# Optimization experiments

Measured on AMD Instinct MI355X. Metric: run time of the kernel, lower is better.

Reference implementation:

```python
import math
import jax, jax.numpy as jnp
import numpy as np

B, T, D, H, FACTOR = 8, 4096, 1024, 16, 5
DH = D // H


def setup_inputs() -> dict:
    key = jax.random.key(0)
    ks = jax.random.split(key, 7)
    u = max(1, min(int(FACTOR * math.log(T + 1)), T))  # = 41
    s = 1.0 / np.sqrt(D).astype(np.float32)
    x = jax.random.normal(ks[0], (B, T, D), jnp.float32)
    Wq = jax.random.normal(ks[1], (D, D), jnp.float32) * s
    Wk = jax.random.normal(ks[2], (D, D), jnp.float32) * s
    Wv = jax.random.normal(ks[3], (D, D), jnp.float32) * s
    Wo = jax.random.normal(ks[4], (D, D), jnp.float32) * s
    bo = jax.random.normal(ks[5], (D,), jnp.float32) * 0.01
    # unique indices, mirroring torch.randperm(T)[:u]
    idx = jax.random.permutation(ks[6], T)[:u].astype(jnp.int32)
    return {"x": x, "Wq": Wq, "Wk": Wk, "Wv": Wv, "Wo": Wo, "bo": bo, "idx": idx}


def reference(x, Wq, Wk, Wv, Wo, bo, idx):
    Bx, Tx, Dx = x.shape
    scale = 1.0 / np.sqrt(DH).astype(np.float32)

    def proj(W):  # torch Linear: x @ W.T, then split heads -> [B,H,T,Dh]
        return (x @ W.T).reshape(Bx, Tx, H, DH).transpose(0, 2, 1, 3)

    Q = proj(Wq)
    K = proj(Wk)
    V = proj(Wv)

    Qs = Q[:, :, idx, :]                                   # [B,H,u,Dh] gather
    scores = jnp.einsum('bhud,bhtd->bhut', Qs, K) * scale  # [B,H,u,T]
    attn = jax.nn.softmax(scores, axis=-1)
    ctx = jnp.einsum('bhut,bhtd->bhud', attn, V)           # [B,H,u,Dh]

    # mean over the u sampled positions fills non-sampled slots
    out = jnp.broadcast_to(ctx.mean(axis=2, keepdims=True), (Bx, H, Tx, DH))
    out = out.at[:, :, idx, :].set(ctx)                    # scatter ctx back

    y = out.transpose(0, 2, 1, 3).reshape(Bx, Tx, Dx)
    return y @ Wo.T + bo
```

## Files before the change

### kernel.cpp

```cpp
#include <hip/hip_runtime.h>
#include <hip/hip_bf16.h>

#define B_  8
#define T_  4096
#define D_  1024
#define H_  16
#define DH_ 64
#define NC_ 4

typedef __bf16 bf8 __attribute__((ext_vector_type(8)));
typedef float f32x4 __attribute__((ext_vector_type(4)));

__device__ __forceinline__ unsigned short f2bf_rn(float f) {
    unsigned u = __float_as_uint(f);
    unsigned r = (u + 0x7FFF + ((u >> 16) & 1)) >> 16;
    return (unsigned short)r;
}

__device__ __forceinline__ void async_load16(const void* gp, void* lp) {
    __builtin_amdgcn_global_load_lds(
        (const __attribute__((address_space(1))) unsigned*)(gp),
        (__attribute__((address_space(3))) unsigned*)(lp), 16, 0, 0);
}

__global__ void k_prep(const float* __restrict__ x, short* __restrict__ xb,
                       const float* __restrict__ Wv, short* __restrict__ Wvb,
                       short* __restrict__ Qtb, const int* __restrict__ idx,
                       int* __restrict__ sel, int U, int HU, int MP, int nzp) {
    int g = blockIdx.x;
    int tid = threadIdx.x;
    if (g < 16896) {
        const float* src = (g < 16384) ? x : Wv;
        short* dst = (g < 16384) ? xb : Wvb;
        size_t gg = (g < 16384) ? g : (g - 16384);
        size_t i = (gg * 256 + tid) * 8;
        float4 a = *(const float4*)(src + i);
        float4 b = *(const float4*)(src + i + 4);
        short4 s0, s1;
        s0.x = (short)f2bf_rn(a.x); s0.y = (short)f2bf_rn(a.y);
        s0.z = (short)f2bf_rn(a.z); s0.w = (short)f2bf_rn(a.w);
        s1.x = (short)f2bf_rn(b.x); s1.y = (short)f2bf_rn(b.y);
        s1.z = (short)f2bf_rn(b.z); s1.w = (short)f2bf_rn(b.w);
        *(short4*)(dst + i) = s0;
        *(short4*)(dst + i + 4) = s1;
    } else if (g < 16896 + nzp) {
        int bi = g - 16896;
        int npad = MP - HU;
        int b = bi / npad, r = bi - b * npad;
        short4 z = {0, 0, 0, 0};
        *(short4*)(Qtb + ((size_t)b * MP + HU + r) * D_ + tid * 4) = z;
    } else {
        for (int t = tid; t < T_; t += 256) sel[t] = 0;
        __syncthreads();
        if (tid < U) sel[idx[tid]] = tid + 1;
    }
}

__global__ __launch_bounds__(256) void k_projg(const float* __restrict__ x,
                                               const int* __restrict__ idx,
                                               const float* __restrict__ W,
                                               float* __restrict__ C, int U) {
    __shared__ float As[32][64 + 4];
    __shared__ float Bs[32][64 + 4];
    __shared__ int sidx[64];
    int M = B_ * U;
    if (threadIdx.x < U) sidx[threadIdx.x] = idx[threadIdx.x];
    __syncthreads();
    int m0 = blockIdx.x * 64, n0 = blockIdx.y * 64;
    int tid = threadIdx.x;
    int lr = tid >> 3, lc = (tid & 7) * 4;
    int ty = tid >> 4, tx = tid & 15;
    float acc[4][4] = {{0.f}};
    for (int k0 = 0; k0 < D_; k0 += 32) {
#pragma unroll
        for (int half = 0; half < 2; ++half) {
            int r = lr + half * 32;
            int gm = m0 + r;
            float4 v = make_float4(0.f, 0.f, 0.f, 0.f);
            if (gm < M) {
                int b = gm / U, i = gm - b * U;
                v = *(const float4*)(x + ((size_t)(b * T_ + sidx[i])) * D_ + k0 + lc);
            }
            As[lc + 0][r] = v.x; As[lc + 1][r] = v.y; As[lc + 2][r] = v.z; As[lc + 3][r] = v.w;
            int gn = n0 + r;
            float4 w = *(const float4*)(W + (size_t)gn * D_ + k0 + lc);
            Bs[lc + 0][r] = w.x; Bs[lc + 1][r] = w.y; Bs[lc + 2][r] = w.z; Bs[lc + 3][r] = w.w;
        }
        __syncthreads();
#pragma unroll
        for (int kk = 0; kk < 32; ++kk) {
            float4 a = *(const float4*)&As[kk][ty * 4];
            float4 bb = *(const float4*)&Bs[kk][tx * 4];
            acc[0][0] += a.x * bb.x; acc[0][1] += a.x * bb.y; acc[0][2] += a.x * bb.z; acc[0][3] += a.x * bb.w;
            acc[1][0] += a.y * bb.x; acc[1][1] += a.y * bb.y; acc[1][2] += a.y * bb.z; acc[1][3] += a.y * bb.w;
            acc[2][0] += a.z * bb.x; acc[2][1] += a.z * bb.y; acc[2][2] += a.z * bb.z; acc[2][3] += a.z * bb.w;
            acc[3][0] += a.w * bb.x; acc[3][1] += a.w * bb.y; acc[3][2] += a.w * bb.z; acc[3][3] += a.w * bb.w;
        }
        __syncthreads();
    }
#pragma unroll
    for (int i = 0; i < 4; ++i) {
        int gm = m0 + ty * 4 + i;
        if (gm < M)
            *(float4*)(C + (size_t)gm * D_ + n0 + tx * 4) =
                make_float4(acc[i][0], acc[i][1], acc[i][2], acc[i][3]);
    }
}

__global__ __launch_bounds__(256) void k_proj(const float* __restrict__ A,
                                              const float* __restrict__ W,
                                              const float* __restrict__ bias,
                                              float* __restrict__ C, int M) {
    __shared__ float As[32][64 + 4];
    __shared__ float Bs[32][64 + 4];
    int m0 = blockIdx.x * 64, n0 = blockIdx.y * 64;
    int tid = threadIdx.x;
    int lr = tid >> 3, lc = (tid & 7) * 4;
    int ty = tid >> 4, tx = tid & 15;
    float acc[4][4] = {{0.f}};
    for (int k0 = 0; k0 < D_; k0 += 32) {
#pragma unroll
        for (int half = 0; half < 2; ++half) {
            int r = lr + half * 32;
            int gm = m0 + r;
            float4 v = make_float4(0.f, 0.f, 0.f, 0.f);
            if (gm < M) v = *(const float4*)(A + (size_t)gm * D_ + k0 + lc);
            As[lc + 0][r] = v.x; As[lc + 1][r] = v.y; As[lc + 2][r] = v.z; As[lc + 3][r] = v.w;
            int gn = n0 + r;
            float4 w = *(const float4*)(W + (size_t)gn * D_ + k0 + lc);
            Bs[lc + 0][r] = w.x; Bs[lc + 1][r] = w.y; Bs[lc + 2][r] = w.z; Bs[lc + 3][r] = w.w;
        }
        __syncthreads();
#pragma unroll
        for (int kk = 0; kk < 32; ++kk) {
            float4 a = *(const float4*)&As[kk][ty * 4];
            float4 bb = *(const float4*)&Bs[kk][tx * 4];
            acc[0][0] += a.x * bb.x; acc[0][1] += a.x * bb.y; acc[0][2] += a.x * bb.z; acc[0][3] += a.x * bb.w;
            acc[1][0] += a.y * bb.x; acc[1][1] += a.y * bb.y; acc[1][2] += a.y * bb.z; acc[1][3] += a.y * bb.w;
            acc[2][0] += a.z * bb.x; acc[2][1] += a.z * bb.y; acc[2][2] += a.z * bb.z; acc[2][3] += a.z * bb.w;
            acc[3][0] += a.w * bb.x; acc[3][1] += a.w * bb.y; acc[3][2] += a.w * bb.z; acc[3][3] += a.w * bb.w;
        }
        __syncthreads();
    }
#pragma unroll
    for (int i = 0; i < 4; ++i) {
        int gm = m0 + ty * 4 + i;
        if (gm < M) {
            int gn = n0 + tx * 4;
            float4 v = make_float4(acc[i][0], acc[i][1], acc[i][2], acc[i][3]);
            if (bias) {
                v.x += bias[gn + 0]; v.y += bias[gn + 1];
                v.z += bias[gn + 2]; v.w += bias[gn + 3];
            }
            *(float4*)(C + (size_t)gm * D_ + gn) = v;
        }
    }
}

__global__ __launch_bounds__(256) void k_qth(const float* __restrict__ Qs,
                                             const float* __restrict__ Wk,
                                             short* __restrict__ Qtb, int U, int MP) {
    __shared__ float As[32][64 + 4];
    __shared__ float Bs[32][64 + 4];
    int h = blockIdx.z;
    int m0 = blockIdx.x * 64, n0 = blockIdx.y * 64;
    int BU = B_ * U;
    int tid = threadIdx.x;
    int lr = tid >> 3, lc = (tid & 7) * 4;
    int ty = tid >> 4, tx = tid & 15;
    float acc[4][4] = {{0.f}};
    for (int k0 = 0; k0 < DH_; k0 += 32) {
#pragma unroll
        for (int half = 0; half < 2; ++half) {
            int r = lr + half * 32;
            int gm = m0 + r;
            float4 v = make_float4(0.f, 0.f, 0.f, 0.f);
            if (gm < BU) v = *(const float4*)(Qs + (size_t)gm * D_ + h * DH_ + k0 + lc);
            As[lc + 0][r] = v.x; As[lc + 1][r] = v.y; As[lc + 2][r] = v.z; As[lc + 3][r] = v.w;
            int kr = (tid >> 4) + half * 16;
            int nc = (tid & 15) * 4;
            float4 w = *(const float4*)(Wk + ((size_t)(h * DH_ + k0 + kr)) * D_ + n0 + nc);
            *(float4*)&Bs[kr][nc] = w;
        }
        __syncthreads();
#pragma unroll
        for (int kk = 0; kk < 32; ++kk) {
            float4 a = *(const float4*)&As[kk][ty * 4];
            float4 bb = *(const float4*)&Bs[kk][tx * 4];
            acc[0][0] += a.x * bb.x; acc[0][1] += a.x * bb.y; acc[0][2] += a.x * bb.z; acc[0][3] += a.x * bb.w;
            acc[1][0] += a.y * bb.x; acc[1][1] += a.y * bb.y; acc[1][2] += a.y * bb.z; acc[1][3] += a.y * bb.w;
            acc[2][0] += a.z * bb.x; acc[2][1] += a.z * bb.y; acc[2][2] += a.z * bb.z; acc[2][3] += a.z * bb.w;
            acc[3][0] += a.w * bb.x; acc[3][1] += a.w * bb.y; acc[3][2] += a.w * bb.z; acc[3][3] += a.w * bb.w;
        }
        __syncthreads();
    }
#pragma unroll
    for (int i = 0; i < 4; ++i) {
        int gm = m0 + ty * 4 + i;
        if (gm < BU) {
            int b = gm / U, ii = gm - b * U;
            short4 s;
            s.x = (short)f2bf_rn(0.125f * acc[i][0]);
            s.y = (short)f2bf_rn(0.125f * acc[i][1]);
            s.z = (short)f2bf_rn(0.125f * acc[i][2]);
            s.w = (short)f2bf_rn(0.125f * acc[i][3]);
            *(short4*)(Qtb + ((size_t)b * MP + h * U + ii) * D_ + n0 + tx * 4) = s;
        }
    }
}

__global__ __launch_bounds__(256) void k_scores_v(const short* __restrict__ Qtb,
                                                  const short* __restrict__ xb,
                                                  const short* __restrict__ Wvb,
                                                  short* __restrict__ attnb,
                                                  short* __restrict__ Vt, int MP) {
    __shared__ short smem[8192];
    short* As = smem;
    short* Bs = smem + 4096;
    int g = blockIdx.x;
    int tid = threadIdx.x;
    int lane = tid & 63, w = tid >> 6;
    int wr = w >> 1, wc = w & 1;
    int quad = lane >> 4, l15 = lane & 15;
    const int K = D_;

    f32x4 acc[4][4];
#pragma unroll
    for (int mi = 0; mi < 4; ++mi)
#pragma unroll
        for (int ni = 0; ni < 4; ++ni)
            acc[mi][ni] = (f32x4){0.f, 0.f, 0.f, 0.f};

    int arow = wr * 64 + l15;
    int brow = wc * 64 + l15;
    int koff = quad * 8;

    if (g < 2048) {
        int mr = g & 7, n = (g >> 3) & 7, mq = g >> 6;
        int m = mq * 8 + mr;
        const short* Ab = xb + (size_t)m * 128 * K;
        const short* Bb = Wvb + (size_t)n * 128 * K;
        for (int kt = 0; kt < K; kt += 32) {
#pragma unroll
            for (int i = 0; i < 2; ++i) {
                int li = i * 256 + tid;
                int row = li >> 2, kc = (li & 3) << 3;
                async_load16(Ab + (size_t)row * K + kt + kc, As + li * 8);
                async_load16(Bb + (size_t)row * K + kt + kc, Bs + li * 8);
            }
            __syncthreads();
            bf8 af[4], bfr[4];
#pragma unroll
            for (int mi = 0; mi < 4; ++mi)
                af[mi] = *(const bf8*)(As + (arow + mi * 16) * 32 + koff);
#pragma unroll
            for (int ni = 0; ni < 4; ++ni)
                bfr[ni] = *(const bf8*)(Bs + (brow + ni * 16) * 32 + koff);
#pragma unroll
            for (int mi = 0; mi < 4; ++mi)
#pragma unroll
                for (int ni = 0; ni < 4; ++ni)
                    acc[mi][ni] = __builtin_amdgcn_mfma_f32_16x16x32_bf16(af[mi], bfr[ni], acc[mi][ni], 0, 0, 0);
            __syncthreads();
        }
        int b = m >> 5;
        int tG0 = (m & 31) * 128 + wr * 64;
        int h = n * 2 + wc;
        short* ep = smem + w * 2048;
        const int PITCH = 80;
#pragma unroll
        for (int ni = 0; ni < 4; ++ni) {
#pragma unroll
            for (int mi = 0; mi < 4; ++mi) {
                short4 s;
                s.x = (short)f2bf_rn(acc[mi][ni][0]);
                s.y = (short)f2bf_rn(acc[mi][ni][1]);
                s.z = (short)f2bf_rn(acc[mi][ni][2]);
                s.w = (short)f2bf_rn(acc[mi][ni][3]);
                *(short4*)(ep + l15 * PITCH + mi * 16 + quad * 4) = s;
            }
#pragma unroll
            for (int it = 0; it < 2; ++it) {
                int dhl = it * 8 + (lane >> 3);
                int seg = lane & 7;
                bf8 v = *(const bf8*)(ep + dhl * PITCH + seg * 8);
                int dh = ni * 16 + dhl;
                *(bf8*)(Vt + ((size_t)(b * H_ + h) * DH_ + dh) * T_ + tG0 + seg * 8) = v;
            }
        }
    } else {
        int gs = g - 2048;
        int n8 = (gs >> 3) & 3;
        int m = (gs >> 5) % 6;
        int b = (gs >> 5) / 6;
        int n = (gs & 7) + 8 * n8;
        const short* Ab = Qtb + (size_t)b * MP * K;
        const short* Bb = xb + (size_t)b * T_ * K;
        short* Cb = attnb + (size_t)b * MP * T_;
        int m0 = m * 128, n0 = n * 128;
        for (int kt = 0; kt < K; kt += 32) {
#pragma unroll
            for (int i = 0; i < 2; ++i) {
                int li = i * 256 + tid;
                int row = li >> 2, kc = (li & 3) << 3;
                async_load16(Ab + (size_t)(m0 + row) * K + kt + kc, As + li * 8);
                async_load16(Bb + (size_t)(n0 + row) * K + kt + kc, Bs + li * 8);
            }
            __syncthreads();
            bf8 af[4], bfr[4];
#pragma unroll
            for (int mi = 0; mi < 4; ++mi)
                af[mi] = *(const bf8*)(As + (arow + mi * 16) * 32 + koff);
#pragma unroll
            for (int ni = 0; ni < 4; ++ni)
                bfr[ni] = *(const bf8*)(Bs + (brow + ni * 16) * 32 + koff);
#pragma unroll
            for (int ni = 0; ni < 4; ++ni)
#pragma unroll
                for (int mi = 0; mi < 4; ++mi)
                    acc[ni][mi] = __builtin_amdgcn_mfma_f32_16x16x32_bf16(bfr[ni], af[mi], acc[ni][mi], 0, 0, 0);
            __syncthreads();
        }
#pragma unroll
        for (int ni = 0; ni < 4; ++ni)
#pragma unroll
            for (int mi = 0; mi < 4; ++mi) {
                int grow = m0 + wr * 64 + mi * 16 + l15;
                int col = n0 + wc * 64 + ni * 16 + quad * 4;
                short4 s;
                s.x = (short)f2bf_rn(__expf(acc[ni][mi][0]));
                s.y = (short)f2bf_rn(__expf(acc[ni][mi][1]));
                s.z = (short)f2bf_rn(__expf(acc[ni][mi][2]));
                s.w = (short)f2bf_rn(__expf(acc[ni][mi][3]));
                *(short4*)(Cb + (size_t)grow * T_ + col) = s;
            }
    }
}

__global__ __launch_bounds__(256) void k_pv(const short* __restrict__ attnb,
                                            const short* __restrict__ Vt,
                                            float* __restrict__ Op,
                                            float* __restrict__ rsp,
                                            int U, int MP) {
    __shared__ short vt[64 * 136];
    int gid = blockIdx.x;
    int c = gid & (NC_ - 1);
    int bh = gid >> 2;
    int h = bh & (H_ - 1);
    int b = bh >> 4;
    int tid = threadIdx.x;
    int lane = tid & 63, w = tid >> 6;
    int quad = lane >> 4;
    const short* Arow = attnb + ((size_t)b * MP + h * U) * T_;
    const short* Vrow = Vt + (size_t)bh * DH_ * T_;

    f32x4 O[3];
#pragma unroll
    for (int mi = 0; mi < 3; ++mi) O[mi] = (f32x4){0.f, 0.f, 0.f, 0.f};
    float rs[3] = {0.f, 0.f, 0.f};

    for (int tt = 0; tt < (T_ / NC_) / 128; ++tt) {
        int t0 = c * (T_ / NC_) + tt * 128;
#pragma unroll
        for (int it = 0; it < 4; ++it) {
            int idx = it * 256 + tid;
            int dh = idx >> 4, seg = idx & 15;
            bf8 v = *(const bf8*)(Vrow + (size_t)dh * T_ + t0 + seg * 8);
            *(bf8*)(vt + dh * 136 + seg * 8) = v;
        }
        __syncthreads();
        bf8 af[3][4];
#pragma unroll
        for (int mi = 0; mi < 3; ++mi)
#pragma unroll
            for (int kf = 0; kf < 4; ++kf)
                af[mi][kf] = *(const bf8*)(Arow + (size_t)(mi * 16 + (lane & 15)) * T_ + t0 + kf * 32 + quad * 8);
        if (w == 0) {
#pragma unroll
            for (int mi = 0; mi < 3; ++mi)
#pragma unroll
                for (int kf = 0; kf < 4; ++kf)
#pragma unroll
                    for (int j = 0; j < 8; ++j) rs[mi] += (float)af[mi][kf][j];
        }
#pragma unroll
        for (int kf = 0; kf < 4; ++kf) {
            bf8 bfr = *(const bf8*)(vt + (w * 16 + (lane & 15)) * 136 + kf * 32 + quad * 8);
#pragma unroll
            for (int mi = 0; mi < 3; ++mi)
                O[mi] = __builtin_amdgcn_mfma_f32_16x16x32_bf16(af[mi][kf], bfr, O[mi], 0, 0, 0);
        }
        __syncthreads();
    }
#pragma unroll
    for (int mi = 0; mi < 3; ++mi)
#pragma unroll
        for (int r = 0; r < 4; ++r)
            Op[((size_t)gid * 48 + mi * 16 + quad * 4 + r) * DH_ + w * 16 + (lane & 15)] = O[mi][r];
    if (w == 0) {
#pragma unroll
        for (int mi = 0; mi < 3; ++mi) {
            rs[mi] += __shfl_xor(rs[mi], 16);
            rs[mi] += __shfl_xor(rs[mi], 32);
            if (quad == 0) rsp[(size_t)gid * 48 + mi * 16 + lane] = rs[mi];
        }
    }
}

__global__ __launch_bounds__(256) void k_rows2(const float* __restrict__ Op,
                                               const float* __restrict__ rsp,
                                               float* __restrict__ R, int U) {
    __shared__ float inv[48];
    __shared__ float msum[4][64];
    int bh = blockIdx.x;
    int b = bh >> 4, h = bh & (H_ - 1);
    int tid = threadIdx.x;
    if (tid < 48) {
        float s = 0.f;
        for (int cc = 0; cc < NC_; ++cc) s += rsp[(size_t)(bh * NC_ + cc) * 48 + tid];
        inv[tid] = 1.f / s;
    }
    __syncthreads();
    int dh = tid & 63, ig = tid >> 6;
    float acc = 0.f;
    for (int p = 0; p < 11; ++p) {
        int i = p * 4 + ig;
        if (i < U) {
            float o = 0.f;
            for (int cc = 0; cc < NC_; ++cc)
                o += Op[((size_t)(bh * NC_ + cc) * 48 + i) * DH_ + dh];
            float v = o * inv[i];
            R[((size_t)b * (U + 1) + 1 + i) * D_ + h * DH_ + dh] = v;
            acc += v;
        }
    }
    msum[ig][dh] = acc;
    __syncthreads();
    if (ig == 0)
        R[((size_t)b * (U + 1)) * D_ + h * DH_ + dh] =
            (msum[0][dh] + msum[1][dh] + msum[2][dh] + msum[3][dh]) / (float)U;
}

__global__ __launch_bounds__(256) void k_fill(const float* __restrict__ Yr,
                                              const int* __restrict__ sel,
                                              float* __restrict__ y, int U) {
    int blk = blockIdx.x;
    int b = blk >> 12, t = blk & (T_ - 1);
    int j = sel[t];
    const float4* src = (const float4*)(Yr + ((size_t)b * (U + 1) + j) * D_);
    float4* dst = (float4*)(y + (size_t)blk * D_);
    dst[threadIdx.x] = src[threadIdx.x];
}

extern "C" void kernel_launch(void* const* d_in, const int* in_sizes, int n_in,
                              void* d_out, int out_size, void* d_ws, size_t ws_size,
                              hipStream_t stream) {
    const float* x  = (const float*)d_in[0];
    const float* Wq = (const float*)d_in[1];
    const float* Wk = (const float*)d_in[2];
    const float* Wv = (const float*)d_in[3];
    const float* Wo = (const float*)d_in[4];
    const float* bo = (const float*)d_in[5];
    const int*  idx = (const int*)d_in[6];
    int U = in_sizes[6];
    int HU = H_ * U;
    int MP = ((HU + 127) / 128) * 128;
    int nzp = B_ * (MP - HU);

    char* w = (char*)d_ws;
    auto alloc = [&](size_t bytes) { char* p = w; w += (bytes + 255) & ~(size_t)255; return p; };

    float* Qs    = (float*)alloc((size_t)B_ * U * D_ * 4);
    short* Qtb   = (short*)alloc((size_t)B_ * MP * D_ * 2);
    short* xb    = (short*)alloc((size_t)B_ * T_ * D_ * 2);
    short* Wvb   = (short*)alloc((size_t)D_ * D_ * 2);
    short* attnb = (short*)alloc((size_t)B_ * MP * T_ * 2);
    short* Vtb   = (short*)alloc((size_t)B_ * D_ * T_ * 2);
    float* Opb   = (float*)alloc((size_t)B_ * H_ * NC_ * 48 * DH_ * 4);
    float* rspb  = (float*)alloc((size_t)B_ * H_ * NC_ * 48 * 4);
    float* R     = (float*)alloc((size_t)B_ * (U + 1) * D_ * 4);
    float* Yr    = (float*)alloc((size_t)B_ * (U + 1) * D_ * 4);
    int*   sel   = (int*)alloc((size_t)T_ * 4);

    k_prep<<<dim3(16896 + nzp + 1), dim3(256), 0, stream>>>(x, xb, Wv, Wvb, Qtb, idx, sel, U, HU, MP, nzp);
    k_projg<<<dim3((B_ * U + 63) / 64, D_ / 64), dim3(256), 0, stream>>>(x, idx, Wq, Qs, U);
    k_qth<<<dim3((B_ * U + 63) / 64, D_ / 64, H_), dim3(256), 0, stream>>>(Qs, Wk, Qtb, U, MP);
    k_scores_v<<<dim3(2048 + 8 * 4 * 6 * B_), dim3(256), 0, stream>>>(Qtb, xb, Wvb, attnb, Vtb, MP);
    k_pv<<<dim3(B_ * H_ * NC_), dim3(256), 0, stream>>>(attnb, Vtb, Opb, rspb, U, MP);
    k_rows2<<<dim3(B_ * H_), dim3(256), 0, stream>>>(Opb, rspb, R, U);
    k_proj<<<dim3((B_ * (U + 1) + 63) / 64, D_ / 64), dim3(256), 0, stream>>>(R, Wo, bo, Yr, B_ * (U + 1));
    k_fill<<<dim3(B_ * T_), dim3(256), 0, stream>>>(Yr, sel, (float*)d_out, U);
}
```

Before: 596.5 us.

## Fuse PV and row normalization into one split-K-per-wave kernel, remap block order

Replaces the chunked k_pv plus k_rows2 pair with a single k_pvT kernel per (batch, head). Its four waves split the 128-wide T tile along K, stage V and P in shared memory, and reduce the partial accumulators and row sums through LDS before writing normalized rows and the mean row directly. This drops one launch and the Op/rsp global round trip. The trade-off is only 128 blocks, down from 512, each walking the full T. It also reorders block indexing in k_scores_v so batch is the fastest-varying index, and changes the epilogue LDS pitch from 80 to 72.

```diff
diff --git a/kernel.cpp b/kernel.cpp
--- a/kernel.cpp
+++ b/kernel.cpp
@@ -6,7 +6,6 @@
 #define D_  1024
 #define H_  16
 #define DH_ 64
-#define NC_ 4
 
 typedef __bf16 bf8 __attribute__((ext_vector_type(8)));
 typedef float f32x4 __attribute__((ext_vector_type(4)));
@@ -236,9 +235,10 @@
     int koff = quad * 8;
 
     if (g < 2048) {
-        int mr = g & 7, n = (g >> 3) & 7, mq = g >> 6;
-        int m = mq * 8 + mr;
-        const short* Ab = xb + (size_t)m * 128 * K;
+        int b = g & 7;
+        int n = (g >> 3) & 7;
+        int mq = g >> 6;
+        const short* Ab = xb + (size_t)(b * 32 + mq) * 128 * K;
         const short* Bb = Wvb + (size_t)n * 128 * K;
         for (int kt = 0; kt < K; kt += 32) {
 #pragma unroll
@@ -263,11 +263,10 @@
                     acc[mi][ni] = __builtin_amdgcn_mfma_f32_16x16x32_bf16(af[mi], bfr[ni], acc[mi][ni], 0, 0, 0);
             __syncthreads();
         }
-        int b = m >> 5;
-        int tG0 = (m & 31) * 128 + wr * 64;
+        int tG0 = mq * 128 + wr * 64;
         int h = n * 2 + wc;
         short* ep = smem + w * 2048;
-        const int PITCH = 80;
+        const int PITCH = 72;
 #pragma unroll
         for (int ni = 0; ni < 4; ++ni) {
 #pragma unroll
@@ -290,10 +289,10 @@
         }
     } else {
         int gs = g - 2048;
-        int n8 = (gs >> 3) & 3;
-        int m = (gs >> 5) % 6;
-        int b = (gs >> 5) / 6;
-        int n = (gs & 7) + 8 * n8;
+        int b = gs & 7;
+        int r2 = gs >> 3;
+        int m = r2 % 6;
+        int n = r2 / 6;
         const short* Ab = Qtb + (size_t)b * MP * K;
         const short* Bb = xb + (size_t)b * T_ * K;
         short* Cb = attnb + (size_t)b * MP * T_;
@@ -337,108 +336,106 @@
     }
 }
 
-__global__ __launch_bounds__(256) void k_pv(const short* __restrict__ attnb,
-                                            const short* __restrict__ Vt,
-                                            float* __restrict__ Op,
-                                            float* __restrict__ rsp,
-                                            int U, int MP) {
-    __shared__ short vt[64 * 136];
+#define VPITCH 136
+__global__ __launch_bounds__(256) void k_pvT(const short* __restrict__ attnb,
+                                             const short* __restrict__ Vt,
+                                             float* __restrict__ R, int U, int MP) {
+    __shared__ short sm[(64 + 48) * VPITCH];
+    __shared__ float redbuf[64 * 48];
+    __shared__ float inv[48];
+    short* vs = sm;
+    short* ps = sm + 64 * VPITCH;
     int gid = blockIdx.x;
-    int c = gid & (NC_ - 1);
-    int bh = gid >> 2;
-    int h = bh & (H_ - 1);
-    int b = bh >> 4;
-    int tid = threadIdx.x;
-    int lane = tid & 63, w = tid >> 6;
-    int quad = lane >> 4;
-    const short* Arow = attnb + ((size_t)b * MP + h * U) * T_;
-    const short* Vrow = Vt + (size_t)bh * DH_ * T_;
-
-    f32x4 O[3];
-#pragma unroll
-    for (int mi = 0; mi < 3; ++mi) O[mi] = (f32x4){0.f, 0.f, 0.f, 0.f};
-    float rs[3] = {0.f, 0.f, 0.f};
-
-    for (int tt = 0; tt < (T_ / NC_) / 128; ++tt) {
-        int t0 = c * (T_ / NC_) + tt * 128;
-#pragma unroll
-        for (int it = 0; it < 4; ++it) {
-            int idx = it * 256 + tid;
-            int dh = idx >> 4, seg = idx & 15;
-            bf8 v = *(const bf8*)(Vrow + (size_t)dh * T_ + t0 + seg * 8);
-            *(bf8*)(vt + dh * 136 + seg * 8) = v;
-        }
-        __syncthreads();
-        bf8 af[3][4];
-#pragma unroll
-        for (int mi = 0; mi < 3; ++mi)
-#pragma unroll
-            for (int kf = 0; kf < 4; ++kf)
-                af[mi][kf] = *(const bf8*)(Arow + (size_t)(mi * 16 + (lane & 15)) * T_ + t0 + kf * 32 + quad * 8);
-        if (w == 0) {
-#pragma unroll
-            for (int mi = 0; mi < 3; ++mi)
-#pragma unroll
-                for (int kf = 0; kf < 4; ++kf)
-#pragma unroll
-                    for (int j = 0; j < 8; ++j) rs[mi] += (float)af[mi][kf][j];
-        }
-#pragma unroll
-        for (int kf = 0; kf < 4; ++kf) {
-            bf8 bfr = *(const bf8*)(vt + (w * 16 + (lane & 15)) * 136 + kf * 32 + quad * 8);
-#pragma unroll
-            for (int mi = 0; mi < 3; ++mi)
-                O[mi] = __builtin_amdgcn_mfma_f32_16x16x32_bf16(af[mi][kf], bfr, O[mi], 0, 0, 0);
-        }
-        __syncthreads();
-    }
-#pragma unroll
-    for (int mi = 0; mi < 3; ++mi)
-#pragma unroll
-        for (int r = 0; r < 4; ++r)
-            Op[((size_t)gid * 48 + mi * 16 + quad * 4 + r) * DH_ + w * 16 + (lane & 15)] = O[mi][r];
-    if (w == 0) {
-#pragma unroll
-        for (int mi = 0; mi < 3; ++mi) {
-            rs[mi] += __shfl_xor(rs[mi], 16);
-            rs[mi] += __shfl_xor(rs[mi], 32);
-            if (quad == 0) rsp[(size_t)gid * 48 + mi * 16 + lane] = rs[mi];
-        }
-    }
-}
-
-__global__ __launch_bounds__(256) void k_rows2(const float* __restrict__ Op,
-                                               const float* __restrict__ rsp,
-                                               float* __restrict__ R, int U) {
-    __shared__ float inv[48];
-    __shared__ float msum[4][64];
-    int bh = blockIdx.x;
-    int b = bh >> 4, h = bh & (H_ - 1);
-    int tid = threadIdx.x;
-    if (tid < 48) {
-        float s = 0.f;
-        for (int cc = 0; cc < NC_; ++cc) s += rsp[(size_t)(bh * NC_ + cc) * 48 + tid];
-        inv[tid] = 1.f / s;
-    }
+    int h = gid & (H_ - 1), b = gid >> 4;
+    int tid = threadIdx.x, lane = tid & 63, w = tid >> 6;
+    int l15 = lane & 15, quad = lane >> 4;
+    const short* Pg = attnb + ((size_t)b * MP + h * U) * T_;
+    const short* Vg = Vt + ((size_t)(b * H_ + h)) * DH_ * T_;
+
+    f32x4 acc[4][3];
+#pragma unroll
+    for (int mf = 0; mf < 4; ++mf)
+#pragma unroll
+        for (int nf = 0; nf < 3; ++nf)
+            acc[mf][nf] = (f32x4){0.f, 0.f, 0.f, 0.f};
+    float rspart = 0.f;
+
+    int vrow = tid >> 2, vseg = tid & 3;
+
+    for (int kt = 0; kt < T_; kt += 128) {
+        {
+            const short* src = Vg + (size_t)vrow * T_ + kt + vseg * 32;
+            short* d = vs + vrow * VPITCH + vseg * 32;
+            bf8 v0 = *(const bf8*)(src);
+            bf8 v1 = *(const bf8*)(src + 8);
+            bf8 v2 = *(const bf8*)(src + 16);
+            bf8 v3 = *(const bf8*)(src + 24);
+            *(bf8*)(d) = v0; *(bf8*)(d + 8) = v1; *(bf8*)(d + 16) = v2; *(bf8*)(d + 24) = v3;
+        }
+        if (tid < 192) {
+            const short* src = Pg + (size_t)vrow * T_ + kt + vseg * 32;
+            short* d = ps + vrow * VPITCH + vseg * 32;
+            bf8 v0 = *(const bf8*)(src);
+            bf8 v1 = *(const bf8*)(src + 8);
+            bf8 v2 = *(const bf8*)(src + 16);
+            bf8 v3 = *(const bf8*)(src + 24);
+            *(bf8*)(d) = v0; *(bf8*)(d + 8) = v1; *(bf8*)(d + 16) = v2; *(bf8*)(d + 24) = v3;
+#pragma unroll
+            for (int j = 0; j < 8; ++j)
+                rspart += (float)v0[j] + (float)v1[j] + (float)v2[j] + (float)v3[j];
+        }
+        __syncthreads();
+        bf8 af[4], bfr[3];
+#pragma unroll
+        for (int mf = 0; mf < 4; ++mf)
+            af[mf] = *(const bf8*)(vs + (mf * 16 + l15) * VPITCH + w * 32 + quad * 8);
+#pragma unroll
+        for (int nf = 0; nf < 3; ++nf)
+            bfr[nf] = *(const bf8*)(ps + (nf * 16 + l15) * VPITCH + w * 32 + quad * 8);
+#pragma unroll
+        for (int mf = 0; mf < 4; ++mf)
+#pragma unroll
+            for (int nf = 0; nf < 3; ++nf)
+                acc[mf][nf] = __builtin_amdgcn_mfma_f32_16x16x32_bf16(af[mf], bfr[nf], acc[mf][nf], 0, 0, 0);
+        __syncthreads();
+    }
+
+    for (int wv = 0; wv < 4; ++wv) {
+        if (w == wv) {
+#pragma unroll
+            for (int mf = 0; mf < 4; ++mf)
+#pragma unroll
+                for (int nf = 0; nf < 3; ++nf)
+#pragma unroll
+                    for (int r = 0; r < 4; ++r) {
+                        int i2 = (mf * 16 + quad * 4 + r) * 48 + nf * 16 + l15;
+                        if (wv == 0) redbuf[i2] = acc[mf][nf][r];
+                        else redbuf[i2] += acc[mf][nf][r];
+                    }
+        }
+        __syncthreads();
+    }
+    float* rsf = (float*)sm;
+    if (tid < 192) rsf[tid] = rspart;
     __syncthreads();
-    int dh = tid & 63, ig = tid >> 6;
-    float acc = 0.f;
-    for (int p = 0; p < 11; ++p) {
-        int i = p * 4 + ig;
-        if (i < U) {
-            float o = 0.f;
-            for (int cc = 0; cc < NC_; ++cc)
-                o += Op[((size_t)(bh * NC_ + cc) * 48 + i) * DH_ + dh];
-            float v = o * inv[i];
-            R[((size_t)b * (U + 1) + 1 + i) * D_ + h * DH_ + dh] = v;
-            acc += v;
-        }
-    }
-    msum[ig][dh] = acc;
+    if (tid < 48)
+        inv[tid] = 1.f / (rsf[tid * 4] + rsf[tid * 4 + 1] + rsf[tid * 4 + 2] + rsf[tid * 4 + 3]);
     __syncthreads();
-    if (ig == 0)
-        R[((size_t)b * (U + 1)) * D_ + h * DH_ + dh] =
-            (msum[0][dh] + msum[1][dh] + msum[2][dh] + msum[3][dh]) / (float)U;
+    int dh = tid >> 2, part = tid & 3;
+    float msum = 0.f;
+#pragma unroll
+    for (int j = 0; j < 12; ++j) {
+        int q = part * 12 + j;
+        if (q < U) {
+            float v = redbuf[dh * 48 + q] * inv[q];
+            R[((size_t)b * (U + 1) + 1 + q) * D_ + h * DH_ + dh] = v;
+            msum += v;
+        }
+    }
+    msum += __shfl_down(msum, 1);
+    msum += __shfl_down(msum, 2);
+    if (part == 0)
+        R[((size_t)b * (U + 1)) * D_ + h * DH_ + dh] = msum / (float)U;
 }
 
 __global__ __launch_bounds__(256) void k_fill(const float* __restrict__ Yr,
@@ -476,8 +473,6 @@
     short* Wvb   = (short*)alloc((size_t)D_ * D_ * 2);
     short* attnb = (short*)alloc((size_t)B_ * MP * T_ * 2);
     short* Vtb   = (short*)alloc((size_t)B_ * D_ * T_ * 2);
-    float* Opb   = (float*)alloc((size_t)B_ * H_ * NC_ * 48 * DH_ * 4);
-    float* rspb  = (float*)alloc((size_t)B_ * H_ * NC_ * 48 * 4);
     float* R     = (float*)alloc((size_t)B_ * (U + 1) * D_ * 4);
     float* Yr    = (float*)alloc((size_t)B_ * (U + 1) * D_ * 4);
     int*   sel   = (int*)alloc((size_t)T_ * 4);
@@ -485,9 +480,8 @@
     k_prep<<<dim3(16896 + nzp + 1), dim3(256), 0, stream>>>(x, xb, Wv, Wvb, Qtb, idx, sel, U, HU, MP, nzp);
     k_projg<<<dim3((B_ * U + 63) / 64, D_ / 64), dim3(256), 0, stream>>>(x, idx, Wq, Qs, U);
     k_qth<<<dim3((B_ * U + 63) / 64, D_ / 64, H_), dim3(256), 0, stream>>>(Qs, Wk, Qtb, U, MP);
-    k_scores_v<<<dim3(2048 + 8 * 4 * 6 * B_), dim3(256), 0, stream>>>(Qtb, xb, Wvb, attnb, Vtb, MP);
-    k_pv<<<dim3(B_ * H_ * NC_), dim3(256), 0, stream>>>(attnb, Vtb, Opb, rspb, U, MP);
-    k_rows2<<<dim3(B_ * H_), dim3(256), 0, stream>>>(Opb, rspb, R, U);
+    k_scores_v<<<dim3(2048 + 1536), dim3(256), 0, stream>>>(Qtb, xb, Wvb, attnb, Vtb, MP);
+    k_pvT<<<dim3(B_ * H_), dim3(256), 0, stream>>>(attnb, Vtb, R, U, MP);
     k_proj<<<dim3((B_ * (U + 1) + 63) / 64, D_ / 64), dim3(256), 0, stream>>>(R, Wo, bo, Yr, B_ * (U + 1));
     k_fill<<<dim3(B_ * T_), dim3(256), 0, stream>>>(Yr, sel, (float*)d_out, U);
 }
```

After: 593.6 us. Within noise of the previous version (-0.5%).
